# Kernel tuning notes

Measured on AMD Instinct MI355X. Metric: run time of the kernel, lower is better.

Reference implementation:

```python
import jax, jax.numpy as jnp
import numpy as np

N_NODES = 100000
N_EDGES = 1600000
D_IN = 128
D_OUT = 128


def setup_inputs() -> dict:
    key = jax.random.key(0)
    k1, k2, k3 = jax.random.split(key, 3)
    x = jax.random.normal(k1, (N_NODES, D_IN), dtype=jnp.float32)
    edge_index = jax.random.randint(k2, (2, N_EDGES), 0, N_NODES, dtype=jnp.int64)
    # glorot-style init for the lazily-created weight
    scale = jnp.sqrt(6.0 / (D_IN + D_OUT)).astype(jnp.float32)
    weight = jax.random.uniform(k3, (D_IN, D_OUT), dtype=jnp.float32, minval=-1.0, maxval=1.0) * scale
    bias = jnp.zeros((D_OUT,), dtype=jnp.float32)
    return {"x": x, "edge_index": edge_index, "weight": weight, "bias": bias}


def reference(x, edge_index, weight, bias):
    N = x.shape[0]
    row, col = edge_index[0], edge_index[1]
    # add_remaining_self_loops: drop existing self-loops (equivalently zero their
    # weight) and append a self-loop of weight 1.0 for every node (improved=False).
    ew = jnp.where(row == col, 0.0, 1.0).astype(x.dtype)
    loop = jnp.arange(N, dtype=row.dtype)
    row = jnp.concatenate([row, loop])
    col = jnp.concatenate([col, loop])
    ew = jnp.concatenate([ew, jnp.ones((N,), dtype=x.dtype)])
    # degree via scatter-add on destination (col), deg^{-1/2} with inf -> 0
    deg = jax.ops.segment_sum(ew, col, num_segments=N)
    deg_inv_sqrt = jnp.where(deg > 0, jax.lax.rsqrt(deg), 0.0).astype(x.dtype)
    norm = deg_inv_sqrt[row] * ew * deg_inv_sqrt[col]  # [E+N]
    # dense transform then gather-scale-scatter (GCN message passing, aggr='add')
    xw = x @ weight  # [N, D_OUT]
    msgs = norm[:, None] * xw[row]  # [E+N, D_OUT] gather on source nodes
    out = jax.ops.segment_sum(msgs, col, num_segments=N)  # scatter-add to dest
    return out + bias
```

## Files before the change

### kernel.cpp

```cpp
#include <hip/hip_runtime.h>
#include <hip/hip_bf16.h>

#define NN 100000
#define NE 1600000
#define D  128
#define NPAD 100352
#define NBLK 782
#define CAP  64

#define BSH    9
#define NB_C   196
#define CAPB   9216
#define PCHUNK 2048
#define PEPT   8
#define NPART  782

typedef __attribute__((ext_vector_type(8))) short short8;
typedef __attribute__((ext_vector_type(4))) float floatx4;

__device__ __forceinline__ unsigned short f2b(float f) {
    __hip_bfloat16 h = __float2bfloat16(f);
    return *(unsigned short*)&h;
}
__device__ __forceinline__ float b2f(unsigned short u) {
    return __uint_as_float(((unsigned)u) << 16);
}

__global__ __launch_bounds__(256) void k_part(const int* __restrict__ row,
                                              const int* __restrict__ col,
                                              int* __restrict__ bcnt,
                                              unsigned int* __restrict__ edgesP) {
    __shared__ int cur[NB_C], basep[NB_C];
    int t = threadIdx.x;
    size_t e0 = (size_t)blockIdx.x * PCHUNK;

    for (int i = t; i < NB_C; i += 256) cur[i] = 0;
    __syncthreads();

    unsigned int val[PEPT];
    int bk[PEPT], rk[PEPT];
#pragma unroll
    for (int i = 0; i < PEPT; ++i) {
        size_t e = e0 + i * 256 + t;
        bk[i] = -1;
        if (e < NE) {
            int r = row[e], c = col[e];
            if (r != c) {
                bk[i]  = c >> BSH;
                val[i] = (unsigned)r | ((unsigned)(c & 511) << 17);
                rk[i]  = atomicAdd(&cur[bk[i]], 1);
            }
        }
    }
    __syncthreads();

    for (int i = t; i < NB_C; i += 256)
        basep[i] = cur[i] ? atomicAdd(&bcnt[i], cur[i]) : 0;
    __syncthreads();

#pragma unroll
    for (int i = 0; i < PEPT; ++i) {
        if (bk[i] >= 0) {
            int pos = basep[bk[i]] + rk[i];
            if (pos < CAPB) edgesP[(size_t)bk[i] * CAPB + pos] = val[i];
        }
    }
}

__global__ __launch_bounds__(256) void k_fine(const int* __restrict__ bcnt,
                                              const unsigned int* __restrict__ edgesP,
                                              int* __restrict__ counts,
                                              float* __restrict__ dinv,
                                              int* __restrict__ srcs) {
    __shared__ int cnt[512];
    int t = threadIdx.x, b = blockIdx.x;
    int n0 = b << BSH;
    for (int i = t; i < 512; i += 256) cnt[i] = 0;
    __syncthreads();

    int m = min(bcnt[b], CAPB);
    const unsigned int* ep = edgesP + (size_t)b * CAPB;
    for (int i = t; i < m; i += 256) {
        unsigned int v = ep[i];
        int c0 = v >> 17;
        int s  = v & 0x1FFFF;
        int pos = atomicAdd(&cnt[c0], 1);
        if (pos < CAP) srcs[(size_t)(n0 + c0) * CAP + pos] = s;
    }
    __syncthreads();
    for (int i = t; i < 512; i += 256) {
        int n = n0 + i;
        int cv = cnt[i];
        counts[n] = min(cv, CAP);
        dinv[n] = rsqrtf((float)cv + 1.0f);
    }
}

__global__ void k_prep_w(const float* __restrict__ w, unsigned short* __restrict__ wt) {
    int i = blockIdx.x * 256 + threadIdx.x;
    int n = i >> 7, k = i & 127;
    wt[i] = f2b(w[k * D + n]);
}

__global__ __launch_bounds__(256, 2) void k_gemm_mfma(const float* __restrict__ x,
                                                      const unsigned short* __restrict__ wt,
                                                      const float* __restrict__ dinv,
                                                      unsigned short* __restrict__ yw) {
    __shared__ unsigned short sX[128 * 128];
    __shared__ unsigned short sW[128 * 128];
    __shared__ float sD[128];
    int tid = threadIdx.x;
    long row0 = (long)blockIdx.x * 128;

    if (tid < 128) {
        long gr = row0 + tid;
        sD[tid] = (gr < NN) ? dinv[gr] : 0.0f;
    }
    {
        const uint4* src = (const uint4*)wt;
        uint4* dst = (uint4*)sW;
#pragma unroll
        for (int j = 0; j < 8; ++j) dst[tid + j * 256] = src[tid + j * 256];
    }
#pragma unroll
    for (int j = 0; j < 16; ++j) {
        int i = tid + j * 256;
        int r = i >> 5, q = i & 31;
        float4 v = make_float4(0.f, 0.f, 0.f, 0.f);
        long gr = row0 + r;
        if (gr < NN) v = *(const float4*)(x + gr * D + q * 4);
        ushort4 u;
        u.x = f2b(v.x); u.y = f2b(v.y); u.z = f2b(v.z); u.w = f2b(v.w);
        *(ushort4*)&sX[r * D + q * 4] = u;
    }
    __syncthreads();

    int lane = tid & 63, wave = tid >> 6;
    int wm = (wave & 1) * 64, wn = (wave >> 1) * 64;
    int lrow = lane & 15, lkb = (lane >> 4) * 8;

    floatx4 acc[4][4] = {};
#pragma unroll
    for (int kc = 0; kc < 4; ++kc) {
        int kb = kc * 32 + lkb;
        short8 bfr[4];
#pragma unroll
        for (int tn = 0; tn < 4; ++tn)
            bfr[tn] = *(const short8*)&sW[(wn + tn * 16 + lrow) * D + kb];
#pragma unroll
        for (int tm = 0; tm < 4; ++tm) {
            short8 afr = *(const short8*)&sX[(wm + tm * 16 + lrow) * D + kb];
#pragma unroll
            for (int tn = 0; tn < 4; ++tn)
                acc[tm][tn] = __builtin_amdgcn_mfma_f32_16x16x32_bf16(afr, bfr[tn], acc[tm][tn], 0, 0, 0);
        }
    }

    int orow = (lane >> 4) * 4;
    int ocol = lane & 15;
#pragma unroll
    for (int tm = 0; tm < 4; ++tm) {
#pragma unroll
        for (int reg = 0; reg < 4; ++reg) {
            int  rt = wm + tm * 16 + orow + reg;
            long m  = row0 + rt;
            if (m < NN) {
                float dm = sD[rt];
                unsigned short* o = yw + m * D + wn + ocol;
#pragma unroll
                for (int tn = 0; tn < 4; ++tn) o[tn * 16] = f2b(acc[tm][tn][reg] * dm);
            }
        }
    }
}

__global__ __launch_bounds__(256) void k_agg(const int* __restrict__ counts,
                                             const int* __restrict__ srcs,
                                             const float* __restrict__ dinv,
                                             const unsigned int* __restrict__ ywp,
                                             const float* __restrict__ bias,
                                             float* __restrict__ out) {
    int lane = threadIdx.x & 63;
    int c = blockIdx.x * 4 + (threadIdx.x >> 6);

    int cnt = counts[c];
    const int* sp = srcs + (size_t)c * CAP;
    int mysrc = (lane < cnt) ? sp[lane] : 0;

    unsigned int u = ywp[(size_t)c * 64 + lane];
    float acc0 = __uint_as_float(u << 16);
    float acc1 = __uint_as_float(u & 0xFFFF0000u);

    int p = 0;
    for (; p + 8 <= cnt; p += 8) {
        unsigned int v[8];
#pragma unroll
        for (int i = 0; i < 8; ++i) {
            int s = __shfl(mysrc, p + i);
            v[i] = ywp[(size_t)s * 64 + lane];
        }
#pragma unroll
        for (int i = 0; i < 8; ++i) {
            acc0 += __uint_as_float(v[i] << 16);
            acc1 += __uint_as_float(v[i] & 0xFFFF0000u);
        }
    }
    for (; p < cnt; ++p) {
        int s = __shfl(mysrc, p);
        unsigned int v = ywp[(size_t)s * 64 + lane];
        acc0 += __uint_as_float(v << 16);
        acc1 += __uint_as_float(v & 0xFFFF0000u);
    }

    float dc = dinv[c];
    float2 b2 = ((const float2*)bias)[lane];
    float2 o;
    o.x = dc * acc0 + b2.x;
    o.y = dc * acc1 + b2.y;
    ((float2*)(out + (size_t)c * D))[lane] = o;
}

extern "C" void kernel_launch(void* const* d_in, const int* in_sizes, int n_in,
                              void* d_out, int out_size, void* d_ws, size_t ws_size,
                              hipStream_t stream) {
    const float* x    = (const float*)d_in[0];
    const int*   ei   = (const int*)d_in[1];
    const float* w    = (const float*)d_in[2];
    const float* bias = (const float*)d_in[3];
    float*       out  = (float*)d_out;

    const int* row = ei;
    const int* col = ei + NE;

    int*   counts = (int*)d_ws;
    float* dinv   = (float*)(counts + NPAD);
    int*   srcs   = (int*)(dinv + NPAD);
    unsigned short* yw = (unsigned short*)(srcs + (size_t)NN * CAP);
    unsigned short* wt = yw + (size_t)NN * D;
    int*   bcnt   = (int*)(wt + 128 * 128);
    unsigned int* edgesP = (unsigned int*)yw;

    hipMemsetAsync(bcnt, 0, NB_C * sizeof(int), stream);

    k_prep_w<<<64, 256, 0, stream>>>(w, wt);
    k_part<<<NPART, 256, 0, stream>>>(row, col, bcnt, edgesP);
    k_fine<<<NB_C, 256, 0, stream>>>(bcnt, edgesP, counts, dinv, srcs);
    k_gemm_mfma<<<NBLK, 256, 0, stream>>>(x, wt, dinv, yw);
    k_agg<<<NN / 4, 256, 0, stream>>>(counts, srcs, dinv, (const unsigned int*)yw, bias, out);
}
```

Before: 242.0 us.

## Slice feature dimension for L2-local aggregation, swizzle GEMM LDS, widen fine-bucketing blocks

The transformed features are now stored in eight 16-column slices, each contiguous over nodes. The aggregation kernel becomes persistent: each block owns one slice, and eight threads per destination node gather 32-bit pairs, so each slice's working set is small enough to stay cache-resident. Source indices are staged through LDS, and outputs and streaming inputs use nontemporal hints. The GEMM LDS tiles get an XOR swizzle to avoid bank conflicts, and the fine-bucketing kernel moves to 1024 threads per block. The risks are scattered 4-byte gathers and less coalesced GEMM output stores.

```diff
diff --git a/kernel.cpp b/kernel.cpp
--- a/kernel.cpp
+++ b/kernel.cpp
@@ -15,15 +15,22 @@
 #define PEPT   8
 #define NPART  782
 
+#define NSL    8
+#define NGRP   3125
+#define AGG_BLOCKS 2048
+
 typedef __attribute__((ext_vector_type(8))) short short8;
 typedef __attribute__((ext_vector_type(4))) float floatx4;
+typedef __attribute__((ext_vector_type(2))) float fx2;
+typedef __attribute__((ext_vector_type(4))) int intx4;
 
 __device__ __forceinline__ unsigned short f2b(float f) {
     __hip_bfloat16 h = __float2bfloat16(f);
     return *(unsigned short*)&h;
 }
-__device__ __forceinline__ float b2f(unsigned short u) {
-    return __uint_as_float(((unsigned)u) << 16);
+
+__device__ __forceinline__ int swz(int row, int col_us) {
+    return row * 128 + (col_us ^ ((row & 7) << 3));
 }
 
 __global__ __launch_bounds__(256) void k_part(const int* __restrict__ row,
@@ -67,20 +74,20 @@
     }
 }
 
-__global__ __launch_bounds__(256) void k_fine(const int* __restrict__ bcnt,
-                                              const unsigned int* __restrict__ edgesP,
-                                              int* __restrict__ counts,
-                                              float* __restrict__ dinv,
-                                              int* __restrict__ srcs) {
+__global__ __launch_bounds__(1024) void k_fine(const int* __restrict__ bcnt,
+                                               const unsigned int* __restrict__ edgesP,
+                                               int* __restrict__ counts,
+                                               float* __restrict__ dinv,
+                                               int* __restrict__ srcs) {
     __shared__ int cnt[512];
     int t = threadIdx.x, b = blockIdx.x;
     int n0 = b << BSH;
-    for (int i = t; i < 512; i += 256) cnt[i] = 0;
+    for (int i = t; i < 512; i += 1024) cnt[i] = 0;
     __syncthreads();
 
     int m = min(bcnt[b], CAPB);
     const unsigned int* ep = edgesP + (size_t)b * CAPB;
-    for (int i = t; i < m; i += 256) {
+    for (int i = t; i < m; i += 1024) {
         unsigned int v = ep[i];
         int c0 = v >> 17;
         int s  = v & 0x1FFFF;
@@ -88,7 +95,7 @@
         if (pos < CAP) srcs[(size_t)(n0 + c0) * CAP + pos] = s;
     }
     __syncthreads();
-    for (int i = t; i < 512; i += 256) {
+    for (int i = t; i < 512; i += 1024) {
         int n = n0 + i;
         int cv = cnt[i];
         counts[n] = min(cv, CAP);
@@ -99,7 +106,7 @@
 __global__ void k_prep_w(const float* __restrict__ w, unsigned short* __restrict__ wt) {
     int i = blockIdx.x * 256 + threadIdx.x;
     int n = i >> 7, k = i & 127;
-    wt[i] = f2b(w[k * D + n]);
+    wt[swz(n, k)] = f2b(w[k * D + n]);
 }
 
 __global__ __launch_bounds__(256, 2) void k_gemm_mfma(const float* __restrict__ x,
@@ -126,12 +133,12 @@
     for (int j = 0; j < 16; ++j) {
         int i = tid + j * 256;
         int r = i >> 5, q = i & 31;
-        float4 v = make_float4(0.f, 0.f, 0.f, 0.f);
+        floatx4 v = {0.f, 0.f, 0.f, 0.f};
         long gr = row0 + r;
-        if (gr < NN) v = *(const float4*)(x + gr * D + q * 4);
+        if (gr < NN) v = __builtin_nontemporal_load((const floatx4*)(x + gr * D + q * 4));
         ushort4 u;
         u.x = f2b(v.x); u.y = f2b(v.y); u.z = f2b(v.z); u.w = f2b(v.w);
-        *(ushort4*)&sX[r * D + q * 4] = u;
+        *(ushort4*)&sX[swz(r, q * 4)] = u;
     }
     __syncthreads();
 
@@ -146,10 +153,10 @@
         short8 bfr[4];
 #pragma unroll
         for (int tn = 0; tn < 4; ++tn)
-            bfr[tn] = *(const short8*)&sW[(wn + tn * 16 + lrow) * D + kb];
+            bfr[tn] = *(const short8*)&sW[swz(wn + tn * 16 + lrow, kb)];
 #pragma unroll
         for (int tm = 0; tm < 4; ++tm) {
-            short8 afr = *(const short8*)&sX[(wm + tm * 16 + lrow) * D + kb];
+            short8 afr = *(const short8*)&sX[swz(wm + tm * 16 + lrow, kb)];
 #pragma unroll
             for (int tn = 0; tn < 4; ++tn)
                 acc[tm][tn] = __builtin_amdgcn_mfma_f32_16x16x32_bf16(afr, bfr[tn], acc[tm][tn], 0, 0, 0);
@@ -158,6 +165,7 @@
 
     int orow = (lane >> 4) * 4;
     int ocol = lane & 15;
+    int wb = wn >> 4;
 #pragma unroll
     for (int tm = 0; tm < 4; ++tm) {
 #pragma unroll
@@ -166,58 +174,83 @@
             long m  = row0 + rt;
             if (m < NN) {
                 float dm = sD[rt];
-                unsigned short* o = yw + m * D + wn + ocol;
-#pragma unroll
-                for (int tn = 0; tn < 4; ++tn) o[tn * 16] = f2b(acc[tm][tn][reg] * dm);
+                unsigned short* o = yw + ((size_t)wb * NN + m) * 16 + ocol;
+#pragma unroll
+                for (int tn = 0; tn < 4; ++tn)
+                    o[(size_t)tn * NN * 16] = f2b(acc[tm][tn][reg] * dm);
             }
         }
     }
 }
 
-__global__ __launch_bounds__(256) void k_agg(const int* __restrict__ counts,
-                                             const int* __restrict__ srcs,
-                                             const float* __restrict__ dinv,
-                                             const unsigned int* __restrict__ ywp,
-                                             const float* __restrict__ bias,
-                                             float* __restrict__ out) {
-    int lane = threadIdx.x & 63;
-    int c = blockIdx.x * 4 + (threadIdx.x >> 6);
-
-    int cnt = counts[c];
-    const int* sp = srcs + (size_t)c * CAP;
-    int mysrc = (lane < cnt) ? sp[lane] : 0;
-
-    unsigned int u = ywp[(size_t)c * 64 + lane];
-    float acc0 = __uint_as_float(u << 16);
-    float acc1 = __uint_as_float(u & 0xFFFF0000u);
-
-    int p = 0;
-    for (; p + 8 <= cnt; p += 8) {
-        unsigned int v[8];
-#pragma unroll
-        for (int i = 0; i < 8; ++i) {
-            int s = __shfl(mysrc, p + i);
-            v[i] = ywp[(size_t)s * 64 + lane];
-        }
-#pragma unroll
-        for (int i = 0; i < 8; ++i) {
-            acc0 += __uint_as_float(v[i] << 16);
-            acc1 += __uint_as_float(v[i] & 0xFFFF0000u);
-        }
-    }
-    for (; p < cnt; ++p) {
-        int s = __shfl(mysrc, p);
-        unsigned int v = ywp[(size_t)s * 64 + lane];
-        acc0 += __uint_as_float(v << 16);
-        acc1 += __uint_as_float(v & 0xFFFF0000u);
-    }
-
-    float dc = dinv[c];
-    float2 b2 = ((const float2*)bias)[lane];
-    float2 o;
-    o.x = dc * acc0 + b2.x;
-    o.y = dc * acc1 + b2.y;
-    ((float2*)(out + (size_t)c * D))[lane] = o;
+__global__ __launch_bounds__(256, 8) void k_agg(const int* __restrict__ counts,
+                                                const int* __restrict__ srcs,
+                                                const float* __restrict__ dinv,
+                                                const unsigned int* __restrict__ ywd,
+                                                const float* __restrict__ bias,
+                                                float* __restrict__ out) {
+    __shared__ int slds[32 * 40];
+    int tid = threadIdx.x;
+    int w = tid >> 6;
+    int d = (tid >> 3) & 7;
+    int j = tid & 7;
+    int din = w * 8 + d;
+    int sl = blockIdx.x & 7;
+
+    const unsigned int* ywj = ywd + (size_t)sl * NN * 8 + j;
+    fx2 b2 = *(const fx2*)(bias + sl * 16 + 2 * j);
+
+    int r = tid >> 3, q = tid & 7;
+
+    for (int grp = blockIdx.x >> 3; grp < NGRP; grp += AGG_BLOCKS / 8) {
+        int c0 = grp * 32;
+        {
+            intx4 v = __builtin_nontemporal_load(
+                (const intx4*)(srcs + (size_t)(c0 + r) * CAP + q * 4));
+            *(intx4*)&slds[r * 40 + q * 4] = v;
+        }
+        __syncthreads();
+
+        int c = c0 + din;
+        int cnt = counts[c];
+        float dc = dinv[c];
+        const int* srow = slds + din * 40;
+
+        unsigned int v0 = ywj[(size_t)c * 8];
+        float a0 = __uint_as_float(v0 << 16);
+        float a1 = __uint_as_float(v0 & 0xFFFF0000u);
+
+        int lim = min(cnt, 32);
+        int p = 0;
+        for (; p + 4 <= lim; p += 4) {
+            intx4 s4 = *(const intx4*)(srow + p);
+            unsigned int g0 = ywj[(size_t)s4.x * 8];
+            unsigned int g1 = ywj[(size_t)s4.y * 8];
+            unsigned int g2 = ywj[(size_t)s4.z * 8];
+            unsigned int g3 = ywj[(size_t)s4.w * 8];
+            a0 += __uint_as_float(g0 << 16);  a1 += __uint_as_float(g0 & 0xFFFF0000u);
+            a0 += __uint_as_float(g1 << 16);  a1 += __uint_as_float(g1 & 0xFFFF0000u);
+            a0 += __uint_as_float(g2 << 16);  a1 += __uint_as_float(g2 & 0xFFFF0000u);
+            a0 += __uint_as_float(g3 << 16);  a1 += __uint_as_float(g3 & 0xFFFF0000u);
+        }
+        for (; p < lim; ++p) {
+            unsigned int g = ywj[(size_t)srow[p] * 8];
+            a0 += __uint_as_float(g << 16);  a1 += __uint_as_float(g & 0xFFFF0000u);
+        }
+        if (cnt > 32) {
+            const int* sp2 = srcs + (size_t)c * CAP;
+            for (p = 32; p < cnt; ++p) {
+                unsigned int g = ywj[(size_t)sp2[p] * 8];
+                a0 += __uint_as_float(g << 16);  a1 += __uint_as_float(g & 0xFFFF0000u);
+            }
+        }
+
+        fx2 o;
+        o.x = dc * a0 + b2.x;
+        o.y = dc * a1 + b2.y;
+        __builtin_nontemporal_store(o, (fx2*)(out + (size_t)c * D + sl * 16 + 2 * j));
+        __syncthreads();
+    }
 }
 
 extern "C" void kernel_launch(void* const* d_in, const int* in_sizes, int n_in,
@@ -244,7 +277,7 @@
 
     k_prep_w<<<64, 256, 0, stream>>>(w, wt);
     k_part<<<NPART, 256, 0, stream>>>(row, col, bcnt, edgesP);
-    k_fine<<<NB_C, 256, 0, stream>>>(bcnt, edgesP, counts, dinv, srcs);
+    k_fine<<<NB_C, 1024, 0, stream>>>(bcnt, edgesP, counts, dinv, srcs);
     k_gemm_mfma<<<NBLK, 256, 0, stream>>>(x, wt, dinv, yw);
-    k_agg<<<NN / 4, 256, 0, stream>>>(counts, srcs, dinv, (const unsigned int*)yw, bias, out);
-}
+    k_agg<<<AGG_BLOCKS, 256, 0, stream>>>(counts, srcs, dinv, (const unsigned int*)yw, bias, out);
+}
```

Result: slower. 260.1 us (+7.4%).
